# Kernel tuning notes

Measured on AMD Instinct MI355X. Metric: run time of the kernel, lower is better.

The kernel has to match this reference:

```python
import jax, jax.numpy as jnp
import numpy as np

N_NODES = 100000
N_EDGES = 3200000


def _gat_conv(x, src, dst, ea, Wx, We, a_src, a_dst, a_edge, b, n):
    # PyG GATConv, heads=1, edge_dim set: h = x@Wx^T, he = ea@We^T
    h = x @ Wx.T                      # [N,16]
    he = ea @ We.T                    # [E,16]
    alpha = h[src] @ a_src + h[dst] @ a_dst + he @ a_edge  # [E]
    alpha = jnp.where(alpha > 0, alpha, 0.2 * alpha)       # leaky_relu(0.2)
    m = jax.ops.segment_max(alpha, dst, num_segments=n)
    m = jnp.where(jnp.isfinite(m), m, 0.0)
    ex = jnp.exp(alpha - m[dst])
    s = jax.ops.segment_sum(ex, dst, num_segments=n)
    a = ex / (s[dst] + 1e-16)
    out = jax.ops.segment_sum(a[:, None] * h[src], dst, num_segments=n)
    return out + b


def setup_inputs() -> dict:
    key = jax.random.key(0)
    ks = iter(jax.random.split(key, 40))
    rn = lambda shape, s=0.1: jax.random.normal(next(ks), shape, dtype=jnp.float32) * s
    inp = {}
    inp['x'] = jax.random.normal(next(ks), (N_NODES, 4), dtype=jnp.float32)
    inp['edge_index'] = jax.random.randint(next(ks), (2, N_EDGES), 0, N_NODES, dtype=jnp.int64)
    inp['edge_attr'] = jax.random.normal(next(ks), (N_EDGES, 6), dtype=jnp.float32)
    # conv1: GATConv(4->16, edge_dim=6)
    inp['c1_Wx'] = rn((16, 4)); inp['c1_We'] = rn((16, 6))
    inp['c1_asrc'] = rn((16,)); inp['c1_adst'] = rn((16,)); inp['c1_aedge'] = rn((16,))
    inp['c1_b'] = rn((16,))
    # edge1 MLP: 38->32->64->32->16
    inp['e1_w1'] = rn((32, 38)); inp['e1_b1'] = rn((32,))
    inp['e1_w2'] = rn((64, 32)); inp['e1_b2'] = rn((64,))
    inp['e1_w3'] = rn((32, 64)); inp['e1_b3'] = rn((32,))
    inp['e1_w4'] = rn((16, 32)); inp['e1_b4'] = rn((16,))
    # conv2: GATConv(16->16, edge_dim=16)
    inp['c2_Wx'] = rn((16, 16)); inp['c2_We'] = rn((16, 16))
    inp['c2_asrc'] = rn((16,)); inp['c2_adst'] = rn((16,)); inp['c2_aedge'] = rn((16,))
    inp['c2_b'] = rn((16,))
    # node head 16->16->2, edge head 16->16->4
    inp['nl_w1'] = rn((16, 16)); inp['nl_b1'] = rn((16,))
    inp['nl_w2'] = rn((2, 16)); inp['nl_b2'] = rn((2,))
    inp['el_w1'] = rn((16, 16)); inp['el_b1'] = rn((16,))
    inp['el_w2'] = rn((4, 16)); inp['el_b2'] = rn((4,))
    return inp


def reference(x, edge_index, edge_attr,
              c1_Wx, c1_We, c1_asrc, c1_adst, c1_aedge, c1_b,
              e1_w1, e1_b1, e1_w2, e1_b2, e1_w3, e1_b3, e1_w4, e1_b4,
              c2_Wx, c2_We, c2_asrc, c2_adst, c2_aedge, c2_b,
              nl_w1, nl_b1, nl_w2, nl_b2,
              el_w1, el_b1, el_w2, el_b2):
    n = x.shape[0]
    src, dst = edge_index[0], edge_index[1]
    x1 = _gat_conv(x, src, dst, edge_attr, c1_Wx, c1_We, c1_asrc, c1_adst, c1_aedge, c1_b, n)
    # edge MLP on [x_src | edge_attr | x_dst] (dropout = identity in eval)
    e = jnp.concatenate([x1[src], edge_attr, x1[dst]], axis=1)  # [E,38]
    e = jax.nn.relu(e @ e1_w1.T + e1_b1)
    e = jax.nn.relu(e @ e1_w2.T + e1_b2)
    e = jax.nn.relu(e @ e1_w3.T + e1_b3)
    e = e @ e1_w4.T + e1_b4                                     # [E,16]
    x2 = _gat_conv(x1, src, dst, e, c2_Wx, c2_We, c2_asrc, c2_adst, c2_aedge, c2_b, n)
    node = jax.nn.relu(jax.nn.relu(x2 @ nl_w1.T + nl_b1) @ nl_w2.T + nl_b2)
    edge = jax.nn.relu(jax.nn.relu(e @ el_w1.T + el_b1) @ el_w2.T + el_b2)
    return (jax.nn.log_softmax(node, axis=1), jax.nn.log_softmax(edge, axis=1))
```

## Files before the change

kernel.cpp:

```cpp
#include <hip/hip_runtime.h>

#define NN 100000
#define NE 3200000
#define NB 98

typedef unsigned int u32;
typedef unsigned short u16;
typedef _Float16 f16x2 __attribute__((ext_vector_type(2)));
typedef __fp16 fp16v2 __attribute__((ext_vector_type(2)));

__device__ __forceinline__ int clampi(int s){
  s = s < 0 ? 0 : s;
  return s >= NN ? NN-1 : s;
}

__device__ __forceinline__ f16x2 pk2(float x, float y){
  fp16v2 r = __builtin_amdgcn_cvt_pkrtz(x, y);
  return __builtin_bit_cast(f16x2, r);
}
__device__ __forceinline__ float dot2(f16x2 a, f16x2 b, float c){
  return __builtin_amdgcn_fdot2(a, b, c, false);
}
__device__ __forceinline__ float f16lo(u32 w){
  __fp16 h = __builtin_bit_cast(__fp16, (u16)(w & 0xffffu));
  return (float)h;
}
__device__ __forceinline__ float f16hi(u32 w){
  __fp16 h = __builtin_bit_cast(__fp16, (u16)(w >> 16));
  return (float)h;
}
__device__ __forceinline__ float f16u(u16 w){
  __fp16 h = __builtin_bit_cast(__fp16, w);
  return (float)h;
}

template<int N4>
__device__ __forceinline__ float dotl(const float* __restrict__ a, const float* w){
  float acc0 = 0.f, acc1 = 0.f;
  #pragma unroll
  for (int k = 0; k < N4; k += 2){
    float4 q0 = ((const float4*)w)[k];
    acc0 += a[4*k]*q0.x + a[4*k+1]*q0.y + a[4*k+2]*q0.z + a[4*k+3]*q0.w;
    float4 q1 = ((const float4*)w)[k+1];
    acc1 += a[4*k+4]*q1.x + a[4*k+5]*q1.y + a[4*k+6]*q1.z + a[4*k+7]*q1.w;
  }
  return acc0 + acc1;
}

__global__ __launch_bounds__(256,8) void khist(const int* __restrict__ ei, int* __restrict__ cnt){
  int i = blockIdx.x*256 + threadIdx.x;
  if (i >= NE) return;
  atomicAdd(&cnt[clampi(ei[NE+i])], 1);
}

__global__ __launch_bounds__(1024) void kscanA(const int* __restrict__ cnt, int* __restrict__ bsum){
  __shared__ int wsum[16];
  int tid = threadIdx.x;
  int i = blockIdx.x*1024 + tid;
  int x = (i < NN) ? cnt[i] : 0;
  #pragma unroll
  for (int ofs = 1; ofs < 64; ofs <<= 1) x += __shfl_xor(x, ofs, 64);
  if ((tid & 63) == 0) wsum[tid >> 6] = x;
  __syncthreads();
  if (tid == 0){
    int t = 0;
    #pragma unroll
    for (int k = 0; k < 16; k++) t += wsum[k];
    bsum[blockIdx.x] = t;
  }
}

__global__ void kscanB(const int* __restrict__ bsum, int* __restrict__ boff, int* __restrict__ offN){
  if (threadIdx.x == 0){
    int c = 0;
    for (int b = 0; b < NB; b++){ boff[b] = c; c += bsum[b]; }
    offN[0] = c;
  }
}

__global__ __launch_bounds__(1024) void kscanC(int* __restrict__ cnt, const int* __restrict__ boff,
                                               int* __restrict__ off){
  __shared__ int wsum[16];
  int tid = threadIdx.x;
  int i = blockIdx.x*1024 + tid;
  int v = (i < NN) ? cnt[i] : 0;
  int x = v;
  #pragma unroll
  for (int ofs = 1; ofs < 64; ofs <<= 1){
    int t = __shfl_up(x, ofs, 64);
    if ((tid & 63) >= ofs) x += t;
  }
  if ((tid & 63) == 63) wsum[tid >> 6] = x;
  __syncthreads();
  if (tid < 16){
    int y = wsum[tid];
    #pragma unroll
    for (int ofs = 1; ofs < 16; ofs <<= 1){
      int t = __shfl_up(y, ofs, 64);
      if (tid >= ofs) y += t;
    }
    wsum[tid] = y;
  }
  __syncthreads();
  int wb = (tid >= 64) ? wsum[(tid >> 6) - 1] : 0;
  if (i < NN){ off[i] = boff[blockIdx.x] + wb + x - v; cnt[i] = 0; }
}

__global__ __launch_bounds__(256,4) void k1(const float* __restrict__ x,
    const float* __restrict__ Wx, const float* __restrict__ asrc, const float* __restrict__ adst,
    u32* __restrict__ hpk, float* __restrict__ hs1, float* __restrict__ hd1)
{
  __shared__ float wL[64], aS[16], aD[16];
  int tid = threadIdx.x;
  if (tid < 64) wL[tid] = Wx[tid];
  if (tid < 16){ aS[tid] = asrc[tid]; aD[tid] = adst[tid]; }
  __syncthreads();
  int n = blockIdx.x*256 + tid;
  if (n >= NN) return;
  float4 xr = ((const float4*)x)[n];
  float hs=0.f, hd=0.f;
  float hv[16];
  #pragma unroll
  for (int j=0;j<16;j++){
    float h = xr.x*wL[j*4+0] + xr.y*wL[j*4+1] + xr.z*wL[j*4+2] + xr.w*wL[j*4+3];
    hv[j] = h; hs += h*aS[j]; hd += h*aD[j];
  }
  u32* hr = hpk + (size_t)n*8;
  #pragma unroll
  for (int j=0;j<8;j++) hr[j] = __builtin_bit_cast(u32, pk2(hv[2*j], hv[2*j+1]));
  hs1[n]=hs; hd1[n]=hd;
}

__global__ __launch_bounds__(256,8) void k2a(const int* __restrict__ ei,
    const float* __restrict__ ea, const float* __restrict__ We, const float* __restrict__ aedge,
    const float* __restrict__ hs1, const float* __restrict__ hd1,
    const int* __restrict__ off, int* __restrict__ cnt, float2* __restrict__ edata)
{
  __shared__ float w6[6];
  int tid = threadIdx.x;
  if (tid < 6){
    float acc = 0.f;
    for (int j=0;j<16;j++) acc += aedge[j] * We[j*6+tid];
    w6[tid] = acc;
  }
  __syncthreads();
  int i = blockIdx.x*256 + tid;
  if (i >= NE) return;
  int s = clampi(ei[i]);
  int d = clampi(ei[NE + i]);
  const float2* eap = (const float2*)ea + (size_t)i*3;
  float2 u0 = eap[0], u1 = eap[1], u2 = eap[2];
  float al = hs1[s] + hd1[d]
    + u0.x*w6[0] + u0.y*w6[1] + u1.x*w6[2]
    + u1.y*w6[3] + u2.x*w6[4] + u2.y*w6[5];
  al = al > 0.f ? al : 0.2f*al;
  float ex = __expf(al);
  int pos = off[d] + atomicAdd(&cnt[d], 1);
  edata[pos] = make_float2(ex, __int_as_float(s));
}

__global__ __launch_bounds__(256,8) void kagg(const float2* __restrict__ edata,
    const int* __restrict__ off, const u16* __restrict__ hpk,
    float* __restrict__ acc, float* __restrict__ s, int* __restrict__ cnt)
{
  int n = (blockIdx.x*256 + threadIdx.x) >> 4;
  int j = threadIdx.x & 15;
  if (n >= NN) return;
  int beg = off[n], end = off[n+1];
  float aj = 0.f, sl = 0.f;
  for (int k = beg; k < end; ++k){
    float2 p = edata[k];
    int src = __float_as_int(p.y);
    aj += p.x * f16u(hpk[(size_t)src*16 + j]);
    sl += p.x;
  }
  acc[(size_t)n*16 + j] = aj;
  if (j == 0){ s[n] = sl; cnt[n] = 0; }
}

__global__ __launch_bounds__(256,2) void k4(const float* __restrict__ accb,
    const float* __restrict__ sb, const float* __restrict__ c1b, const float* __restrict__ Wx2,
    const float* __restrict__ a2s, const float* __restrict__ a2d,
    const float* __restrict__ w1p,
    u32* __restrict__ hpk,
    float* __restrict__ hs2, float* __restrict__ hd2,
    u32* __restrict__ uh, u32* __restrict__ vh)
{
  __shared__ float wL[256], bL[16], aS[16], aD[16];
  __shared__ float w1sL[32*16], w1dL[32*16];
  int tid = threadIdx.x;
  wL[tid] = Wx2[tid];
  if (tid < 16){ bL[tid]=c1b[tid]; aS[tid]=a2s[tid]; aD[tid]=a2d[tid]; }
  for (int idx=tid; idx<512; idx+=256){
    int j=idx>>4, k=idx&15;
    w1sL[idx] = w1p[j*38+k];
    w1dL[idx] = w1p[j*38+22+k];
  }
  __syncthreads();
  int n = blockIdx.x*256 + tid;
  if (n >= NN) return;
  float inv = 1.f/(sb[n] + 1e-16f);
  float xv[16];
  const float* xp = accb + (size_t)n*16;
  #pragma unroll
  for (int j=0;j<16;j++) xv[j] = xp[j]*inv + bL[j];
  float hs=0.f, hd=0.f;
  float hv[16];
  #pragma unroll
  for (int j=0;j<16;j++){
    float acc = 0.f;
    #pragma unroll
    for (int k=0;k<16;k++) acc += xv[k]*wL[j*16+k];
    hv[j] = acc; hs += acc*aS[j]; hd += acc*aD[j];
  }
  u32* hr = hpk + (size_t)n*8;
  #pragma unroll
  for (int j=0;j<8;j++) hr[j] = __builtin_bit_cast(u32, pk2(hv[2*j], hv[2*j+1]));
  hs2[n]=hs; hd2[n]=hd;
  u32* ur = uh + (size_t)n*16;
  u32* vr = vh + (size_t)n*16;
  #pragma unroll
  for (int j=0;j<16;j++){
    float u0 = dotl<4>(xv, &w1sL[(2*j)*16]);
    float u1 = dotl<4>(xv, &w1sL[(2*j+1)*16]);
    ur[j] = __builtin_bit_cast(u32, pk2(u0, u1));
    float v0 = dotl<4>(xv, &w1dL[(2*j)*16]);
    float v1 = dotl<4>(xv, &w1dL[(2*j+1)*16]);
    vr[j] = __builtin_bit_cast(u32, pk2(v0, v1));
  }
}

__global__ __launch_bounds__(256,5) void k5(
    const int* __restrict__ ei, const float* __restrict__ ea,
    const u32* __restrict__ uh, const u32* __restrict__ vh,
    const float* __restrict__ hs2, const float* __restrict__ hd2,
    const float* w1p, const float* b1p, const float* w2p, const float* b2p,
    const float* w3p, const float* b3p, const float* w4p, const float* b4p,
    const float* We2, const float* a2e,
    const float* ew1p, const float* eb1p, const float* ew2p, const float* eb2p,
    const int* __restrict__ off, int* __restrict__ cnt, float2* __restrict__ edata,
    float* __restrict__ eout)
{
  __shared__ __align__(16) f16x2 w1eh[32*4];  __shared__ float b1L[32];
  __shared__ __align__(16) f16x2 w2h[64*16];  __shared__ float b2L[64];
  __shared__ __align__(16) f16x2 w3h[32*32];  __shared__ float b3L[32];
  __shared__ __align__(16) f16x2 w4h[16*16];  __shared__ float b4L[16];
  __shared__ __align__(16) f16x2 ew1h[16*8];  __shared__ float eb1L[16];
  __shared__ __align__(16) f16x2 ew2h[4*8];   __shared__ float eb2L[4];
  __shared__ __align__(16) f16x2 w16h[8];
  int tid = threadIdx.x;
  if (tid < 128){
    int j=tid>>2, kk=tid&3;
    int k0=2*kk, k1=2*kk+1;
    float v0 = (k0<6) ? w1p[j*38+16+k0] : 0.f;
    float v1 = (k1<6) ? w1p[j*38+16+k1] : 0.f;
    w1eh[tid] = pk2(v0, v1);
  }
  for (int idx=tid; idx<1024; idx+=256){
    int j=idx>>4, kk=idx&15;
    w2h[idx] = pk2(w2p[j*32+2*kk], w2p[j*32+2*kk+1]);
  }
  for (int idx=tid; idx<1024; idx+=256){
    int j=idx>>5, kk=idx&31;
    w3h[idx] = pk2(w3p[j*64+2*kk], w3p[j*64+2*kk+1]);
  }
  if (tid < 256){
    int j=tid>>4, kk=tid&15;
    w4h[tid] = pk2(w4p[j*32+2*kk], w4p[j*32+2*kk+1]);
  }
  if (tid < 128){
    int j=tid>>3, kk=tid&7;
    ew1h[tid] = pk2(ew1p[j*16+2*kk], ew1p[j*16+2*kk+1]);
  }
  if (tid < 32){
    int j=tid>>3, kk=tid&7;
    ew2h[tid] = pk2(ew2p[j*16+2*kk], ew2p[j*16+2*kk+1]);
  }
  if (tid < 8){
    float s0=0.f, s1=0.f;
    for (int j=0;j<16;j++){
      s0 += a2e[j] * We2[j*16 + 2*tid];
      s1 += a2e[j] * We2[j*16 + 2*tid + 1];
    }
    w16h[tid] = pk2(s0, s1);
  }
  if (tid < 64) b2L[tid] = b2p[tid];
  if (tid < 32){ b1L[tid] = b1p[tid]; b3L[tid] = b3p[tid]; }
  if (tid < 16){ b4L[tid] = b4p[tid]; eb1L[tid] = eb1p[tid]; }
  if (tid < 4)  eb2L[tid] = eb2p[tid];
  __syncthreads();

  int i = blockIdx.x*256 + tid;
  if (i >= NE) return;
  int s = clampi(ei[i]);
  int d = clampi(ei[NE + i]);

  f16x2 a1h[16];
  {
    const float2* eap = (const float2*)ea + (size_t)i*3;
    float2 e0=eap[0], e1=eap[1], e2=eap[2];
    f16x2 eh[4];
    eh[0]=pk2(e0.x,e0.y); eh[1]=pk2(e1.x,e1.y); eh[2]=pk2(e2.x,e2.y); eh[3]=pk2(0.f,0.f);
    const uint4* up = (const uint4*)(uh + (size_t)s*16);
    const uint4* vp = (const uint4*)(vh + (size_t)d*16);
    uint4 U[4], V[4];
    #pragma unroll
    for (int q=0;q<4;q++){ U[q]=up[q]; V[q]=vp[q]; }
    u32 uw[16], vw[16];
    #pragma unroll
    for (int q=0;q<4;q++){
      uw[4*q]=U[q].x; uw[4*q+1]=U[q].y; uw[4*q+2]=U[q].z; uw[4*q+3]=U[q].w;
      vw[4*q]=V[q].x; vw[4*q+1]=V[q].y; vw[4*q+2]=V[q].z; vw[4*q+3]=V[q].w;
    }
    #pragma unroll
    for (int j=0;j<16;j++){
      float t0 = b1L[2*j]   + f16lo(uw[j]) + f16lo(vw[j]);
      float t1 = b1L[2*j+1] + f16hi(uw[j]) + f16hi(vw[j]);
      #pragma unroll
      for (int kk=0;kk<4;kk++){
        t0 = dot2(eh[kk], w1eh[(2*j)*4+kk],   t0);
        t1 = dot2(eh[kk], w1eh[(2*j+1)*4+kk], t1);
      }
      a1h[j] = pk2(fmaxf(t0,0.f), fmaxf(t1,0.f));
    }
  }
  f16x2 a2h[32];
  #pragma unroll
  for (int j=0;j<32;j++){
    float acc0 = b2L[2*j], acc1 = b2L[2*j+1];
    #pragma unroll
    for (int kk=0;kk<16;kk++){
      acc0 = dot2(a1h[kk], w2h[(2*j)*16+kk],   acc0);
      acc1 = dot2(a1h[kk], w2h[(2*j+1)*16+kk], acc1);
    }
    a2h[j] = pk2(fmaxf(acc0,0.f), fmaxf(acc1,0.f));
  }
  f16x2 a3h[16];
  #pragma unroll
  for (int j=0;j<16;j++){
    float acc0 = b3L[2*j], acc1 = b3L[2*j+1];
    #pragma unroll
    for (int kk=0;kk<32;kk++){
      acc0 = dot2(a2h[kk], w3h[(2*j)*32+kk],   acc0);
      acc1 = dot2(a2h[kk], w3h[(2*j+1)*32+kk], acc1);
    }
    a3h[j] = pk2(fmaxf(acc0,0.f), fmaxf(acc1,0.f));
  }
  f16x2 eh4[8];
  #pragma unroll
  for (int j=0;j<8;j++){
    float acc0 = b4L[2*j], acc1 = b4L[2*j+1];
    #pragma unroll
    for (int kk=0;kk<16;kk++){
      acc0 = dot2(a3h[kk], w4h[(2*j)*16+kk],   acc0);
      acc1 = dot2(a3h[kk], w4h[(2*j+1)*16+kk], acc1);
    }
    eh4[j] = pk2(acc0, acc1);
  }
  f16x2 th[8];
  #pragma unroll
  for (int j=0;j<8;j++){
    float acc0 = eb1L[2*j], acc1 = eb1L[2*j+1];
    #pragma unroll
    for (int kk=0;kk<8;kk++){
      acc0 = dot2(eh4[kk], ew1h[(2*j)*8+kk],   acc0);
      acc1 = dot2(eh4[kk], ew1h[(2*j+1)*8+kk], acc1);
    }
    th[j] = pk2(fmaxf(acc0,0.f), fmaxf(acc1,0.f));
  }
  float y0 = eb2L[0], y1 = eb2L[1], y2 = eb2L[2], y3 = eb2L[3];
  #pragma unroll
  for (int kk=0;kk<8;kk++){
    y0 = dot2(th[kk], ew2h[0*8+kk], y0);
    y1 = dot2(th[kk], ew2h[1*8+kk], y1);
    y2 = dot2(th[kk], ew2h[2*8+kk], y2);
    y3 = dot2(th[kk], ew2h[3*8+kk], y3);
  }
  y0 = fmaxf(y0,0.f); y1 = fmaxf(y1,0.f); y2 = fmaxf(y2,0.f); y3 = fmaxf(y3,0.f);
  float m = fmaxf(fmaxf(y0,y1), fmaxf(y2,y3));
  float l = m + __logf(__expf(y0-m)+__expf(y1-m)+__expf(y2-m)+__expf(y3-m));
  float4 eo; eo.x = y0-l; eo.y = y1-l; eo.z = y2-l; eo.w = y3-l;
  ((float4*)eout)[i] = eo;

  float al = hs2[s] + hd2[d];
  #pragma unroll
  for (int kk=0;kk<8;kk++) al = dot2(eh4[kk], w16h[kk], al);
  al = al > 0.f ? al : 0.2f*al;
  float ex = __expf(al);
  int pos = off[d] + atomicAdd(&cnt[d], 1);
  edata[pos] = make_float2(ex, __int_as_float(s));
}

__global__ __launch_bounds__(256,4) void k7(const float* __restrict__ accb,
    const float* __restrict__ sb, const float* __restrict__ c2b,
    const float* __restrict__ w1p, const float* __restrict__ b1p,
    const float* __restrict__ w2p, const float* __restrict__ b2p,
    float* __restrict__ nout)
{
  __shared__ float wL[256], bL[16], w2L[32], b2L[2], cb[16];
  int tid = threadIdx.x;
  wL[tid] = w1p[tid];
  if (tid < 16){ bL[tid]=b1p[tid]; cb[tid]=c2b[tid]; }
  if (tid < 32) w2L[tid] = w2p[tid];
  if (tid < 2)  b2L[tid] = b2p[tid];
  __syncthreads();
  int n = blockIdx.x*256 + tid;
  if (n >= NN) return;
  float inv = 1.f/(sb[n] + 1e-16f);
  const float* xp = accb + (size_t)n*16;
  float v[16];
  #pragma unroll
  for (int j=0;j<16;j++) v[j] = xp[j]*inv + cb[j];
  float t[16];
  #pragma unroll
  for (int j=0;j<16;j++){
    float acc = bL[j];
    #pragma unroll
    for (int k=0;k<16;k++) acc += v[k]*wL[j*16+k];
    t[j] = fmaxf(acc, 0.f);
  }
  float y0 = b2L[0], y1 = b2L[1];
  #pragma unroll
  for (int k=0;k<16;k++){ y0 += t[k]*w2L[k]; y1 += t[k]*w2L[16+k]; }
  y0 = fmaxf(y0, 0.f); y1 = fmaxf(y1, 0.f);
  float m = fmaxf(y0, y1);
  float l = m + __logf(__expf(y0-m) + __expf(y1-m));
  float2 no; no.x = y0-l; no.y = y1-l;
  ((float2*)nout)[n] = no;
}

extern "C" void kernel_launch(void* const* d_in, const int* in_sizes, int n_in,
                              void* d_out, int out_size, void* d_ws, size_t ws_size,
                              hipStream_t stream)
{
  const float* x  = (const float*)d_in[0];
  const int* ei   = (const int*)d_in[1];
  const float* ea = (const float*)d_in[2];
  const float* c1Wx = (const float*)d_in[3];
  const float* c1We = (const float*)d_in[4];
  const float* c1as = (const float*)d_in[5];
  const float* c1ad = (const float*)d_in[6];
  const float* c1ae = (const float*)d_in[7];
  const float* c1b  = (const float*)d_in[8];
  const float* e1w1 = (const float*)d_in[9];
  const float* e1b1 = (const float*)d_in[10];
  const float* e1w2 = (const float*)d_in[11];
  const float* e1b2 = (const float*)d_in[12];
  const float* e1w3 = (const float*)d_in[13];
  const float* e1b3 = (const float*)d_in[14];
  const float* e1w4 = (const float*)d_in[15];
  const float* e1b4 = (const float*)d_in[16];
  const float* c2Wx = (const float*)d_in[17];
  const float* c2We = (const float*)d_in[18];
  const float* c2as = (const float*)d_in[19];
  const float* c2ad = (const float*)d_in[20];
  const float* c2ae = (const float*)d_in[21];
  const float* c2b  = (const float*)d_in[22];
  const float* nlw1 = (const float*)d_in[23];
  const float* nlb1 = (const float*)d_in[24];
  const float* nlw2 = (const float*)d_in[25];
  const float* nlb2 = (const float*)d_in[26];
  const float* elw1 = (const float*)d_in[27];
  const float* elb1 = (const float*)d_in[28];
  const float* elw2 = (const float*)d_in[29];
  const float* elb2 = (const float*)d_in[30];

  float* ws = (float*)d_ws;
  const size_t N = NN;
  int* off   = (int*)ws;
  int* cnt   = (int*)ws + (N + 8);
  int* bsum  = (int*)ws + (2*N + 8);
  int* boff  = (int*)ws + (2*N + 136);
  u32* hpk   = (u32*)(ws + 2*N + 264);
  float* hs  = ws + 10*N + 264;
  float* hd  = hs + N;
  float* acc = hd + N;
  float* s   = acc + 16*N;
  u32* uh    = (u32*)(s + N);
  u32* vh    = uh + 16*N;
  float2* edata = (float2*)(vh + 16*N);

  float* nout = (float*)d_out;
  float* eout = (float*)d_out + 200000;

  const int GE = (NE + 255)/256;
  const int GN = (NN + 255)/256;

  (void)hipMemsetAsync(cnt, 0, N*sizeof(int), stream);
  khist<<<GE, 256, 0, stream>>>(ei, cnt);
  kscanA<<<NB, 1024, 0, stream>>>(cnt, bsum);
  kscanB<<<1, 64, 0, stream>>>(bsum, boff, off + NN);
  kscanC<<<NB, 1024, 0, stream>>>(cnt, boff, off);
  k1<<<GN, 256, 0, stream>>>(x, c1Wx, c1as, c1ad, hpk, hs, hd);
  k2a<<<GE, 256, 0, stream>>>(ei, ea, c1We, c1ae, hs, hd, off, cnt, edata);
  kagg<<<(NN+15)/16, 256, 0, stream>>>(edata, off, (const u16*)hpk, acc, s, cnt);
  k4<<<GN, 256, 0, stream>>>(acc, s, c1b, c2Wx, c2as, c2ad, e1w1, hpk, hs, hd, uh, vh);
  k5<<<GE, 256, 0, stream>>>(ei, ea, uh, vh, hs, hd,
      e1w1, e1b1, e1w2, e1b2, e1w3, e1b3, e1w4, e1b4,
      c2We, c2ae, elw1, elb1, elw2, elb2,
      off, cnt, edata, eout);
  kagg<<<(NN+15)/16, 256, 0, stream>>>(edata, off, (const u16*)hpk, acc, s, cnt);
  k7<<<GN, 256, 0, stream>>>(acc, s, c2b, nlw1, nlb1, nlw2, nlb2, nout);
}
```

Measured before the change: 803.6 us.

## Aggregate raw 4-dim inputs in first GAT layer and split edge loop across lanes

The first aggregation now sums attention-weighted raw 4-float node features instead of 16-dim projected features, and the projection by Wx is applied after normalization in k4 (linearity). This removes the fp16 h buffer write in k1 and shrinks the gather per edge. The second aggregation uses 64 lanes per node, with four edge-strided groups combined by shuffles, to expose more parallelism for the gather. It also changes rounding slightly, since the first layer now aggregates fp32 inputs instead of fp16 h.

Result: faster. 745.2 us (-7.3%).

```diff
diff --git a/kernel.cpp b/kernel.cpp
--- a/kernel.cpp
+++ b/kernel.cpp
@@ -108,7 +108,7 @@
 
 __global__ __launch_bounds__(256,4) void k1(const float* __restrict__ x,
     const float* __restrict__ Wx, const float* __restrict__ asrc, const float* __restrict__ adst,
-    u32* __restrict__ hpk, float* __restrict__ hs1, float* __restrict__ hd1)
+    float* __restrict__ hs1, float* __restrict__ hd1)
 {
   __shared__ float wL[64], aS[16], aD[16];
   int tid = threadIdx.x;
@@ -119,15 +119,11 @@
   if (n >= NN) return;
   float4 xr = ((const float4*)x)[n];
   float hs=0.f, hd=0.f;
-  float hv[16];
   #pragma unroll
   for (int j=0;j<16;j++){
     float h = xr.x*wL[j*4+0] + xr.y*wL[j*4+1] + xr.z*wL[j*4+2] + xr.w*wL[j*4+3];
-    hv[j] = h; hs += h*aS[j]; hd += h*aD[j];
-  }
-  u32* hr = hpk + (size_t)n*8;
-  #pragma unroll
-  for (int j=0;j<8;j++) hr[j] = __builtin_bit_cast(u32, pk2(hv[2*j], hv[2*j+1]));
+    hs += h*aS[j]; hd += h*aD[j];
+  }
   hs1[n]=hs; hd1[n]=hd;
 }
 
@@ -159,37 +155,66 @@
   edata[pos] = make_float2(ex, __int_as_float(s));
 }
 
-__global__ __launch_bounds__(256,8) void kagg(const float2* __restrict__ edata,
+__global__ __launch_bounds__(256,8) void kaggx(const float2* __restrict__ edata,
+    const int* __restrict__ off, const float* __restrict__ x,
+    float* __restrict__ acc4, float* __restrict__ s, int* __restrict__ cnt)
+{
+  int t = blockIdx.x*256 + threadIdx.x;
+  int n = t >> 4;
+  int j = t & 15;
+  if (n >= NN) return;
+  int f = j & 3, ks = j >> 2;
+  int beg = off[n], end = off[n+1];
+  float aj = 0.f, sl = 0.f;
+  for (int k = beg + ks; k < end; k += 4){
+    float2 p = edata[k];
+    int src = __float_as_int(p.y);
+    aj += p.x * x[(size_t)src*4 + f];
+    sl += p.x;
+  }
+  aj += __shfl_xor(aj, 4, 64); aj += __shfl_xor(aj, 8, 64);
+  sl += __shfl_xor(sl, 4, 64); sl += __shfl_xor(sl, 8, 64);
+  if (ks == 0) acc4[(size_t)n*4 + f] = aj;
+  if (j == 0){ s[n] = sl; cnt[n] = 0; }
+}
+
+__global__ __launch_bounds__(256,8) void kagg2(const float2* __restrict__ edata,
     const int* __restrict__ off, const u16* __restrict__ hpk,
     float* __restrict__ acc, float* __restrict__ s, int* __restrict__ cnt)
 {
-  int n = (blockIdx.x*256 + threadIdx.x) >> 4;
-  int j = threadIdx.x & 15;
+  int t = blockIdx.x*256 + threadIdx.x;
+  int n = t >> 6;
+  int l = t & 63;
   if (n >= NN) return;
+  int j = l & 15, ks = l >> 4;
   int beg = off[n], end = off[n+1];
   float aj = 0.f, sl = 0.f;
-  for (int k = beg; k < end; ++k){
+  for (int k = beg + ks; k < end; k += 4){
     float2 p = edata[k];
     int src = __float_as_int(p.y);
     aj += p.x * f16u(hpk[(size_t)src*16 + j]);
     sl += p.x;
   }
-  acc[(size_t)n*16 + j] = aj;
-  if (j == 0){ s[n] = sl; cnt[n] = 0; }
-}
-
-__global__ __launch_bounds__(256,2) void k4(const float* __restrict__ accb,
-    const float* __restrict__ sb, const float* __restrict__ c1b, const float* __restrict__ Wx2,
+  aj += __shfl_xor(aj, 16, 64); aj += __shfl_xor(aj, 32, 64);
+  sl += __shfl_xor(sl, 16, 64); sl += __shfl_xor(sl, 32, 64);
+  if (ks == 0) acc[(size_t)n*16 + j] = aj;
+  if (l == 0){ s[n] = sl; cnt[n] = 0; }
+}
+
+__global__ __launch_bounds__(256,2) void k4(const float* __restrict__ acc4,
+    const float* __restrict__ sb, const float* __restrict__ c1b,
+    const float* __restrict__ Wx1, const float* __restrict__ Wx2,
     const float* __restrict__ a2s, const float* __restrict__ a2d,
     const float* __restrict__ w1p,
     u32* __restrict__ hpk,
     float* __restrict__ hs2, float* __restrict__ hd2,
     u32* __restrict__ uh, u32* __restrict__ vh)
 {
-  __shared__ float wL[256], bL[16], aS[16], aD[16];
+  __shared__ float wL[256], bL[16], aS[16], aD[16], w0L[64];
   __shared__ float w1sL[32*16], w1dL[32*16];
   int tid = threadIdx.x;
   wL[tid] = Wx2[tid];
+  if (tid < 64) w0L[tid] = Wx1[tid];
   if (tid < 16){ bL[tid]=c1b[tid]; aS[tid]=a2s[tid]; aD[tid]=a2d[tid]; }
   for (int idx=tid; idx<512; idx+=256){
     int j=idx>>4, k=idx&15;
@@ -200,10 +225,12 @@
   int n = blockIdx.x*256 + tid;
   if (n >= NN) return;
   float inv = 1.f/(sb[n] + 1e-16f);
+  float4 a4 = ((const float4*)acc4)[n];
+  float m0 = a4.x*inv, m1 = a4.y*inv, m2 = a4.z*inv, m3 = a4.w*inv;
   float xv[16];
-  const float* xp = accb + (size_t)n*16;
-  #pragma unroll
-  for (int j=0;j<16;j++) xv[j] = xp[j]*inv + bL[j];
+  #pragma unroll
+  for (int j=0;j<16;j++)
+    xv[j] = m0*w0L[j*4+0] + m1*w0L[j*4+1] + m2*w0L[j*4+2] + m3*w0L[j*4+3] + bL[j];
   float hs=0.f, hd=0.f;
   float hv[16];
   #pragma unroll
@@ -475,7 +502,8 @@
   float* hs  = ws + 10*N + 264;
   float* hd  = hs + N;
   float* acc = hd + N;
-  float* s   = acc + 16*N;
+  float* acc4= acc + 16*N;
+  float* s   = acc4 + 4*N;
   u32* uh    = (u32*)(s + N);
   u32* vh    = uh + 16*N;
   float2* edata = (float2*)(vh + 16*N);
@@ -491,14 +519,14 @@
   kscanA<<<NB, 1024, 0, stream>>>(cnt, bsum);
   kscanB<<<1, 64, 0, stream>>>(bsum, boff, off + NN);
   kscanC<<<NB, 1024, 0, stream>>>(cnt, boff, off);
-  k1<<<GN, 256, 0, stream>>>(x, c1Wx, c1as, c1ad, hpk, hs, hd);
+  k1<<<GN, 256, 0, stream>>>(x, c1Wx, c1as, c1ad, hs, hd);
   k2a<<<GE, 256, 0, stream>>>(ei, ea, c1We, c1ae, hs, hd, off, cnt, edata);
-  kagg<<<(NN+15)/16, 256, 0, stream>>>(edata, off, (const u16*)hpk, acc, s, cnt);
-  k4<<<GN, 256, 0, stream>>>(acc, s, c1b, c2Wx, c2as, c2ad, e1w1, hpk, hs, hd, uh, vh);
+  kaggx<<<(NN*16 + 255)/256, 256, 0, stream>>>(edata, off, x, acc4, s, cnt);
+  k4<<<GN, 256, 0, stream>>>(acc4, s, c1b, c1Wx, c2Wx, c2as, c2ad, e1w1, hpk, hs, hd, uh, vh);
   k5<<<GE, 256, 0, stream>>>(ei, ea, uh, vh, hs, hd,
       e1w1, e1b1, e1w2, e1b2, e1w3, e1b3, e1w4, e1b4,
       c2We, c2ae, elw1, elb1, elw2, elb2,
       off, cnt, edata, eout);
-  kagg<<<(NN+15)/16, 256, 0, stream>>>(edata, off, (const u16*)hpk, acc, s, cnt);
+  kagg2<<<(NN*64 + 255)/256, 256, 0, stream>>>(edata, off, (const u16*)hpk, acc, s, cnt);
   k7<<<GN, 256, 0, stream>>>(acc, s, c2b, nlw1, nlb1, nlw2, nlb2, nout);
 }
```
